# Performance work log

Measured on AMD Instinct MI355X. Metric: run time of the kernel, lower is better.

Reference implementation:

```python
import jax, jax.numpy as jnp
import numpy as np

N_NODES = 10000
N_EDGES = 640000
D_IN = 128
D_MODEL = 128


def _gcn_conv(x, W, b, row, col, norm, n):
    # PyG GCNConv: out = scatter_add(norm * (x W)[row] -> col) + b
    h = x @ W  # [N, d_out]
    msg = h[row] * norm[:, None]  # [E+N, d_out] gather + scale
    out = jax.ops.segment_sum(msg, col, num_segments=n)  # scatter-add
    return out + b


def _norm_with_self_loops(row, col, n):
    # add self loops, compute D^-1/2 (A+I) D^-1/2 edge weights
    loops = jnp.arange(n, dtype=row.dtype)
    row_sl = jnp.concatenate([row, loops])
    col_sl = jnp.concatenate([col, loops])
    deg = jax.ops.segment_sum(jnp.ones_like(col_sl, dtype=jnp.float32), col_sl, num_segments=n)
    dis = jnp.where(deg > 0, jax.lax.rsqrt(jnp.maximum(deg, 1.0)), 0.0)
    norm = dis[row_sl] * dis[col_sl]
    return row_sl, col_sl, norm


def setup_inputs() -> dict:
    key = jax.random.key(0)
    k1, k2, k3, k4 = jax.random.split(key, 4)
    glorot1 = (6.0 / (D_IN + D_MODEL)) ** 0.5
    glorot2 = (6.0 / (D_MODEL + D_MODEL)) ** 0.5
    return {
        "x": jax.random.normal(k1, (N_NODES, D_IN), dtype=jnp.float32),
        "edge_index": jax.random.randint(k2, (2, N_EDGES), 0, N_NODES, dtype=jnp.int32),
        "W1": jax.random.uniform(k3, (D_IN, D_MODEL), jnp.float32, -glorot1, glorot1),
        "b1": jnp.zeros((D_MODEL,), jnp.float32),
        "W2": jax.random.uniform(k4, (D_MODEL, D_MODEL), jnp.float32, -glorot2, glorot2),
        "b2": jnp.zeros((D_MODEL,), jnp.float32),
    }


def reference(x, edge_index, W1, b1, W2, b2):
    n = x.shape[0]
    row, col = edge_index[0], edge_index[1]
    row_sl, col_sl, norm = _norm_with_self_loops(row, col, n)
    x1 = jax.nn.relu(_gcn_conv(x, W1, b1, row_sl, col_sl, norm, n))
    x2 = _gcn_conv(x1, W2, b2, row_sl, col_sl, norm, n)
    return (x2, x1)
```

## Files before the change

### kernel.cpp

```cpp
#include <hip/hip_runtime.h>

#define N_NODES 10000
#define N_EDGES 640000
#define D 128
#define NBUCK 157
#define BSTRIDE 160
#define CAP 4608
#define EPT 20
#define BWG 125

__device__ __forceinline__ float asf(unsigned int u) {
    union { unsigned int i; float f; } v; v.i = u; return v.f;
}
__device__ __forceinline__ unsigned int f2bf(float f) {
    union { float f; unsigned int i; } v; v.f = f;
    return (v.i + 0x7fffu + ((v.i >> 16) & 1u)) >> 16;
}

__global__ __launch_bounds__(256) void k_zero_small(int* __restrict__ slab_cnt,
                                                    int* __restrict__ gcur) {
    int t = threadIdx.x;
    if (t < BSTRIDE) slab_cnt[t] = 0;
    if (t == 0) gcur[0] = 0;
}

__global__ __launch_bounds__(256) void k_bucket(const int* __restrict__ row,
                                                const int* __restrict__ col,
                                                int* __restrict__ slab_cnt,
                                                unsigned int* __restrict__ bucketed) {
    __shared__ int hist[BSTRIDE];
    __shared__ int base_s[BSTRIDE];
    int tid = threadIdx.x;
    if (tid < BSTRIDE) hist[tid] = 0;
    __syncthreads();

    int e0 = blockIdx.x * (256 * EPT) + tid;
    unsigned int word[EPT];
    int rank[EPT];
#pragma unroll
    for (int u = 0; u < EPT; ++u) {
        int e = e0 + u * 256;
        int r = row[e];
        int c = col[e];
        word[u] = (unsigned int)r | ((unsigned int)c << 14);
        rank[u] = atomicAdd(&hist[c >> 6], 1);
    }
    __syncthreads();
    if (tid < NBUCK) base_s[tid] = atomicAdd(&slab_cnt[tid], hist[tid]);
    __syncthreads();
#pragma unroll
    for (int u = 0; u < EPT; ++u) {
        int bkt = (int)(word[u] >> 20);
        int idx = base_s[bkt] + rank[u];
        if (idx < CAP) bucketed[(size_t)bkt * CAP + idx] = word[u];
    }
}

__global__ __launch_bounds__(256) void k_place(const unsigned int* __restrict__ bucketed,
                                               const int* __restrict__ slab_cnt,
                                               int* __restrict__ gcur,
                                               int* __restrict__ sorted_row,
                                               int2* __restrict__ node_be,
                                               float* __restrict__ dis) {
    __shared__ int hist[64];
    __shared__ int start[64];
    __shared__ int cur[64];
    __shared__ int baseS;
    int b = blockIdx.x;
    int tid = threadIdx.x;
    if (tid < 64) hist[tid] = 0;
    __syncthreads();

    int scnt = slab_cnt[b];
    if (scnt > CAP) scnt = CAP;
    const unsigned int* slab = bucketed + (size_t)b * CAP;

    for (int k = tid; k < scnt; k += 256) {
        int cl = (int)(slab[k] >> 14) & 63;
        atomicAdd(&hist[cl], 1);
    }
    __syncthreads();

    if (tid < 64) {
        int v = hist[tid];
        int pre = v;
#pragma unroll
        for (int off = 1; off < 64; off <<= 1) {
            int o = __shfl_up(pre, off);
            if (tid >= off) pre += o;
        }
        start[tid] = pre - v;
        if (tid == 63) baseS = atomicAdd(gcur, pre);
    }
    __syncthreads();
    int base = baseS;
    if (tid < 64) {
        int c = (b << 6) + tid;
        if (c < N_NODES) {
            int beg = base + start[tid];
            node_be[c] = make_int2(beg, beg + hist[tid]);
            dis[c] = rsqrtf((float)(hist[tid] + 1));
        }
        cur[tid] = start[tid];
    }
    __syncthreads();

    for (int k = tid; k < scnt; k += 256) {
        unsigned int w = slab[k];
        int cl = (int)(w >> 14) & 63;
        int r = (int)(w & 0x3FFFu);
        int p = atomicAdd(&cur[cl], 1);
        sorted_row[base + p] = r;
    }
}

#define FMA4(acc, s, w)                    \
    acc.x = fmaf(s, w.x, acc.x);           \
    acc.y = fmaf(s, w.y, acc.y);           \
    acc.z = fmaf(s, w.z, acc.z);           \
    acc.w = fmaf(s, w.w, acc.w);

__global__ __launch_bounds__(256) void k_gemm_scale(const float* __restrict__ in,
                                                    const float* __restrict__ W,
                                                    const float* __restrict__ dis,
                                                    uint2* __restrict__ h2) {
    __shared__ float4 sW[128 * 16];
    const float4* W4 = (const float4*)W;
    int half = blockIdx.x & 1;
    int tile = blockIdx.x >> 1;
    int cx = threadIdx.x;
    int ty = threadIdx.y;
    int tid = ty * 16 + cx;
    for (int i = tid; i < 128 * 16; i += 256) {
        int k = i >> 4, q = i & 15;
        sW[i] = W4[k * 32 + half * 16 + q];
    }
    __syncthreads();

    int r0 = tile * 32 + ty * 2;
    if (r0 >= N_NODES) return;

    const float4* xr = (const float4*)(in + (size_t)r0 * D);
    float4 acc0 = {0, 0, 0, 0}, acc1 = {0, 0, 0, 0};

#pragma unroll 4
    for (int k4 = 0; k4 < 32; ++k4) {
        float4 a0 = xr[k4];
        float4 a1 = xr[32 + k4];
        float4 w;
        w = sW[(k4 * 4 + 0) * 16 + cx];
        FMA4(acc0, a0.x, w) FMA4(acc1, a1.x, w)
        w = sW[(k4 * 4 + 1) * 16 + cx];
        FMA4(acc0, a0.y, w) FMA4(acc1, a1.y, w)
        w = sW[(k4 * 4 + 2) * 16 + cx];
        FMA4(acc0, a0.z, w) FMA4(acc1, a1.z, w)
        w = sW[(k4 * 4 + 3) * 16 + cx];
        FMA4(acc0, a0.w, w) FMA4(acc1, a1.w, w)
    }

#pragma unroll
    for (int j = 0; j < 2; ++j) {
        float ds = dis[r0 + j];
        float4 a = j ? acc1 : acc0;
        uint2 o;
        o.x = f2bf(a.x * ds) | (f2bf(a.y * ds) << 16);
        o.y = f2bf(a.z * ds) | (f2bf(a.w * ds) << 16);
        h2[(size_t)(r0 + j) * 32 + half * 16 + cx] = o;
    }
}

__global__ __launch_bounds__(256) void k_gather(const uint4* __restrict__ h4,
                                                const int2* __restrict__ node_be,
                                                const int* __restrict__ sorted_row,
                                                const float* __restrict__ dis,
                                                const float* __restrict__ b,
                                                float* __restrict__ out, int relu) {
    int wave = threadIdx.x >> 6;
    int lane = threadIdx.x & 63;
    int c = blockIdx.x * 4 + wave;
    int g = lane >> 3;
    int l8 = lane & 7;

    float acc[16];
#pragma unroll
    for (int k = 0; k < 16; ++k) acc[k] = 0.f;

#define LOADROW(r, wa, wb)                                  \
    {                                                       \
        const uint4* p = &h4[(size_t)(r) * 16 + l8 * 2];    \
        wa = p[0]; wb = p[1];                               \
    }
#define ACCUM(wa, wb)                                                    \
    {                                                                    \
        acc[0]  += asf(wa.x << 16); acc[1]  += asf(wa.x & 0xffff0000u);  \
        acc[2]  += asf(wa.y << 16); acc[3]  += asf(wa.y & 0xffff0000u);  \
        acc[4]  += asf(wa.z << 16); acc[5]  += asf(wa.z & 0xffff0000u);  \
        acc[6]  += asf(wa.w << 16); acc[7]  += asf(wa.w & 0xffff0000u);  \
        acc[8]  += asf(wb.x << 16); acc[9]  += asf(wb.x & 0xffff0000u);  \
        acc[10] += asf(wb.y << 16); acc[11] += asf(wb.y & 0xffff0000u);  \
        acc[12] += asf(wb.z << 16); acc[13] += asf(wb.z & 0xffff0000u);  \
        acc[14] += asf(wb.w << 16); acc[15] += asf(wb.w & 0xffff0000u);  \
    }

    if (g == 0) {
        uint4 s0, s1;
        LOADROW(c, s0, s1);
        ACCUM(s0, s1);
    }

    int2 be = node_be[c];
    int end = be.y;
    int j = be.x + g;
    if (j < end) {
        int r_cur = sorted_row[j];
        uint4 c0, c1;
        LOADROW(r_cur, c0, c1);
        int j1 = j + 8;
        int r_nxt = (j1 < end) ? sorted_row[j1] : 0;
        while (j1 < end) {
            int j2 = j1 + 8;
            int r_nn = (j2 < end) ? sorted_row[j2] : 0;
            uint4 n0, n1;
            LOADROW(r_nxt, n0, n1);
            ACCUM(c0, c1);
            c0 = n0; c1 = n1;
            r_nxt = r_nn;
            j1 = j2;
        }
        ACCUM(c0, c1);
    }
#undef LOADROW
#undef ACCUM

#pragma unroll
    for (int k = 0; k < 16; ++k) {
        acc[k] += __shfl_xor(acc[k], 8);
        acc[k] += __shfl_xor(acc[k], 16);
        acc[k] += __shfl_xor(acc[k], 32);
    }

    if (g == 0) {
        float ds = dis[c];
        const float4* b4 = (const float4*)b;
        float4* op = (float4*)(out + (size_t)c * D + l8 * 16);
#pragma unroll
        for (int q = 0; q < 4; ++q) {
            float4 bb = b4[l8 * 4 + q];
            float4 o;
            o.x = fmaf(ds, acc[q * 4 + 0], bb.x);
            o.y = fmaf(ds, acc[q * 4 + 1], bb.y);
            o.z = fmaf(ds, acc[q * 4 + 2], bb.z);
            o.w = fmaf(ds, acc[q * 4 + 3], bb.w);
            if (relu) {
                o.x = fmaxf(o.x, 0.f); o.y = fmaxf(o.y, 0.f);
                o.z = fmaxf(o.z, 0.f); o.w = fmaxf(o.w, 0.f);
            }
            op[q] = o;
        }
    }
}

extern "C" void kernel_launch(void* const* d_in, const int* in_sizes, int n_in,
                              void* d_out, int out_size, void* d_ws, size_t ws_size,
                              hipStream_t stream) {
    const float* x  = (const float*)d_in[0];
    const int*   ei = (const int*)d_in[1];
    const float* W1 = (const float*)d_in[2];
    const float* b1 = (const float*)d_in[3];
    const float* W2 = (const float*)d_in[4];
    const float* b2 = (const float*)d_in[5];

    float* out = (float*)d_out;
    float* x2 = out;
    float* x1 = out + (size_t)N_NODES * D;

    const int* row = ei;
    const int* col = ei + N_EDGES;

    int* slab_cnt       = (int*)d_ws;
    int* gcur           = slab_cnt + BSTRIDE;
    float* dis          = (float*)(gcur + 16);
    int2* node_be       = (int2*)(dis + 10016);
    unsigned int* bucketed = (unsigned int*)(node_be + 10016);
    int* sorted_row     = (int*)(bucketed + (size_t)NBUCK * CAP);
    unsigned int* h     = (unsigned int*)(sorted_row + N_EDGES);

    k_zero_small<<<1, 256, 0, stream>>>(slab_cnt, gcur);
    k_bucket<<<BWG, 256, 0, stream>>>(row, col, slab_cnt, bucketed);
    k_place<<<NBUCK, 256, 0, stream>>>(bucketed, slab_cnt, gcur, sorted_row, node_be, dis);

    k_gemm_scale<<<626, dim3(16, 16), 0, stream>>>(x, W1, dis, (uint2*)h);
    k_gather<<<N_NODES / 4, 256, 0, stream>>>((const uint4*)h, node_be, sorted_row, dis, b1, x1, 1);
    k_gemm_scale<<<626, dim3(16, 16), 0, stream>>>(x1, W2, dis, (uint2*)h);
    k_gather<<<N_NODES / 4, 256, 0, stream>>>((const uint4*)h, node_be, sorted_row, dis, b2, x2, 0);
}
```

Baseline: 152.8 us.

## Fuse CSR build with first GEMM and drop global atomics in bucketing

```diff
diff --git a/kernel.cpp b/kernel.cpp
--- a/kernel.cpp
+++ b/kernel.cpp
@@ -6,8 +6,9 @@
 #define NBUCK 157
 #define BSTRIDE 160
 #define CAP 4608
-#define EPT 20
+#define CAP_BB 80
 #define BWG 125
+#define SLOTS (BWG * CAP_BB)
 
 __device__ __forceinline__ float asf(unsigned int u) {
     union { unsigned int i; float f; } v; v.i = u; return v.f;
@@ -17,100 +18,38 @@
     return (v.i + 0x7fffu + ((v.i >> 16) & 1u)) >> 16;
 }
 
-__global__ __launch_bounds__(256) void k_zero_small(int* __restrict__ slab_cnt,
-                                                    int* __restrict__ gcur) {
-    int t = threadIdx.x;
-    if (t < BSTRIDE) slab_cnt[t] = 0;
-    if (t == 0) gcur[0] = 0;
-}
-
-__global__ __launch_bounds__(256) void k_bucket(const int* __restrict__ row,
-                                                const int* __restrict__ col,
-                                                int* __restrict__ slab_cnt,
+__global__ __launch_bounds__(256) void k_bucket(const int4* __restrict__ row4,
+                                                const int4* __restrict__ col4,
+                                                unsigned short* __restrict__ cnt_bb,
                                                 unsigned int* __restrict__ bucketed) {
     __shared__ int hist[BSTRIDE];
-    __shared__ int base_s[BSTRIDE];
     int tid = threadIdx.x;
     if (tid < BSTRIDE) hist[tid] = 0;
     __syncthreads();
 
-    int e0 = blockIdx.x * (256 * EPT) + tid;
-    unsigned int word[EPT];
-    int rank[EPT];
-#pragma unroll
-    for (int u = 0; u < EPT; ++u) {
-        int e = e0 + u * 256;
-        int r = row[e];
-        int c = col[e];
-        word[u] = (unsigned int)r | ((unsigned int)c << 14);
-        rank[u] = atomicAdd(&hist[c >> 6], 1);
-    }
-    __syncthreads();
-    if (tid < NBUCK) base_s[tid] = atomicAdd(&slab_cnt[tid], hist[tid]);
-    __syncthreads();
-#pragma unroll
-    for (int u = 0; u < EPT; ++u) {
+    int base4 = blockIdx.x * 1280;
+    unsigned int word[20];
+    int rank[20];
+#pragma unroll
+    for (int u = 0; u < 5; ++u) {
+        int4 r = row4[base4 + u * 256 + tid];
+        int4 c = col4[base4 + u * 256 + tid];
+        int e = u * 4;
+        word[e+0] = (unsigned)r.x | ((unsigned)c.x << 14); rank[e+0] = atomicAdd(&hist[c.x >> 6], 1);
+        word[e+1] = (unsigned)r.y | ((unsigned)c.y << 14); rank[e+1] = atomicAdd(&hist[c.y >> 6], 1);
+        word[e+2] = (unsigned)r.z | ((unsigned)c.z << 14); rank[e+2] = atomicAdd(&hist[c.z >> 6], 1);
+        word[e+3] = (unsigned)r.w | ((unsigned)c.w << 14); rank[e+3] = atomicAdd(&hist[c.w >> 6], 1);
+    }
+    __syncthreads();
+    if (tid < NBUCK) {
+        int h = hist[tid];
+        cnt_bb[tid * 128 + blockIdx.x] = (unsigned short)(h < CAP_BB ? h : CAP_BB);
+    }
+#pragma unroll
+    for (int u = 0; u < 20; ++u) {
         int bkt = (int)(word[u] >> 20);
-        int idx = base_s[bkt] + rank[u];
-        if (idx < CAP) bucketed[(size_t)bkt * CAP + idx] = word[u];
-    }
-}
-
-__global__ __launch_bounds__(256) void k_place(const unsigned int* __restrict__ bucketed,
-                                               const int* __restrict__ slab_cnt,
-                                               int* __restrict__ gcur,
-                                               int* __restrict__ sorted_row,
-                                               int2* __restrict__ node_be,
-                                               float* __restrict__ dis) {
-    __shared__ int hist[64];
-    __shared__ int start[64];
-    __shared__ int cur[64];
-    __shared__ int baseS;
-    int b = blockIdx.x;
-    int tid = threadIdx.x;
-    if (tid < 64) hist[tid] = 0;
-    __syncthreads();
-
-    int scnt = slab_cnt[b];
-    if (scnt > CAP) scnt = CAP;
-    const unsigned int* slab = bucketed + (size_t)b * CAP;
-
-    for (int k = tid; k < scnt; k += 256) {
-        int cl = (int)(slab[k] >> 14) & 63;
-        atomicAdd(&hist[cl], 1);
-    }
-    __syncthreads();
-
-    if (tid < 64) {
-        int v = hist[tid];
-        int pre = v;
-#pragma unroll
-        for (int off = 1; off < 64; off <<= 1) {
-            int o = __shfl_up(pre, off);
-            if (tid >= off) pre += o;
-        }
-        start[tid] = pre - v;
-        if (tid == 63) baseS = atomicAdd(gcur, pre);
-    }
-    __syncthreads();
-    int base = baseS;
-    if (tid < 64) {
-        int c = (b << 6) + tid;
-        if (c < N_NODES) {
-            int beg = base + start[tid];
-            node_be[c] = make_int2(beg, beg + hist[tid]);
-            dis[c] = rsqrtf((float)(hist[tid] + 1));
-        }
-        cur[tid] = start[tid];
-    }
-    __syncthreads();
-
-    for (int k = tid; k < scnt; k += 256) {
-        unsigned int w = slab[k];
-        int cl = (int)(w >> 14) & 63;
-        int r = (int)(w & 0x3FFFu);
-        int p = atomicAdd(&cur[cl], 1);
-        sorted_row[base + p] = r;
+        if (rank[u] < CAP_BB)
+            bucketed[(size_t)bkt * SLOTS + blockIdx.x * CAP_BB + rank[u]] = word[u];
     }
 }
 
@@ -120,17 +59,18 @@
     acc.z = fmaf(s, w.z, acc.z);           \
     acc.w = fmaf(s, w.w, acc.w);
 
-__global__ __launch_bounds__(256) void k_gemm_scale(const float* __restrict__ in,
-                                                    const float* __restrict__ W,
-                                                    const float* __restrict__ dis,
-                                                    uint2* __restrict__ h2) {
-    __shared__ float4 sW[128 * 16];
+template <bool SCALE>
+__device__ __forceinline__ void gemm_body(int gb, int tid,
+                                          const float* __restrict__ in,
+                                          const float* __restrict__ W,
+                                          const float* __restrict__ dis,
+                                          uint2* __restrict__ h2,
+                                          float4* sW) {
     const float4* W4 = (const float4*)W;
-    int half = blockIdx.x & 1;
-    int tile = blockIdx.x >> 1;
-    int cx = threadIdx.x;
-    int ty = threadIdx.y;
-    int tid = ty * 16 + cx;
+    int half = gb & 1;
+    int tile = gb >> 1;
+    int cx = tid & 15;
+    int ty = tid >> 4;
     for (int i = tid; i < 128 * 16; i += 256) {
         int k = i >> 4, q = i & 15;
         sW[i] = W4[k * 32 + half * 16 + q];
@@ -142,7 +82,6 @@
 
     const float4* xr = (const float4*)(in + (size_t)r0 * D);
     float4 acc0 = {0, 0, 0, 0}, acc1 = {0, 0, 0, 0};
-
 #pragma unroll 4
     for (int k4 = 0; k4 < 32; ++k4) {
         float4 a0 = xr[k4];
@@ -157,24 +96,95 @@
         w = sW[(k4 * 4 + 3) * 16 + cx];
         FMA4(acc0, a0.w, w) FMA4(acc1, a1.w, w)
     }
-
 #pragma unroll
     for (int j = 0; j < 2; ++j) {
-        float ds = dis[r0 + j];
         float4 a = j ? acc1 : acc0;
         uint2 o;
-        o.x = f2bf(a.x * ds) | (f2bf(a.y * ds) << 16);
-        o.y = f2bf(a.z * ds) | (f2bf(a.w * ds) << 16);
+        if (SCALE) {
+            float ds = dis[r0 + j];
+            o.x = f2bf(a.x * ds) | (f2bf(a.y * ds) << 16);
+            o.y = f2bf(a.z * ds) | (f2bf(a.w * ds) << 16);
+        } else {
+            o.x = f2bf(a.x) | (f2bf(a.y) << 16);
+            o.y = f2bf(a.z) | (f2bf(a.w) << 16);
+        }
         h2[(size_t)(r0 + j) * 32 + half * 16 + cx] = o;
     }
 }
 
+__global__ __launch_bounds__(256) void k_fused1(const unsigned int* __restrict__ bucketed,
+                                                const unsigned short* __restrict__ cnt_bb,
+                                                int* __restrict__ sorted_row,
+                                                int2* __restrict__ node_be,
+                                                float* __restrict__ dis,
+                                                const float* __restrict__ x,
+                                                const float* __restrict__ W1,
+                                                uint2* __restrict__ h2) {
+    __shared__ __align__(16) char smem[32768];
+    int tid = threadIdx.x;
+    if (blockIdx.x >= NBUCK) {
+        gemm_body<false>(blockIdx.x - NBUCK, tid, x, W1, nullptr, h2, (float4*)smem);
+        return;
+    }
+    int* hist = (int*)smem;
+    int* cur  = hist + 64;
+    unsigned short* cnt_l = (unsigned short*)(cur + 64);
+    int b = blockIdx.x;
+    if (tid < 64) hist[tid] = 0;
+    if (tid < BWG) cnt_l[tid] = cnt_bb[b * 128 + tid];
+    __syncthreads();
+
+    const unsigned int* slab = bucketed + (size_t)b * SLOTS;
+    for (int k = tid; k < SLOTS; k += 256) {
+        int blk = k / CAP_BB;
+        int idx = k - blk * CAP_BB;
+        if (idx < (int)cnt_l[blk]) {
+            unsigned int w = slab[k];
+            atomicAdd(&hist[(w >> 14) & 63], 1);
+        }
+    }
+    __syncthreads();
+    if (tid < 64) {
+        int v = hist[tid], pre = v;
+#pragma unroll
+        for (int off = 1; off < 64; off <<= 1) {
+            int o = __shfl_up(pre, off);
+            if (tid >= off) pre += o;
+        }
+        cur[tid] = pre - v;
+        int c = (b << 6) + tid;
+        if (c < N_NODES) {
+            node_be[c] = make_int2(b * CAP + pre - v, b * CAP + pre);
+            dis[c] = rsqrtf((float)(v + 1));
+        }
+    }
+    __syncthreads();
+    for (int k = tid; k < SLOTS; k += 256) {
+        int blk = k / CAP_BB;
+        int idx = k - blk * CAP_BB;
+        if (idx < (int)cnt_l[blk]) {
+            unsigned int w = slab[k];
+            int p = atomicAdd(&cur[(w >> 14) & 63], 1);
+            sorted_row[b * CAP + p] = (int)(w & 0x3FFFu);
+        }
+    }
+}
+
+__global__ __launch_bounds__(256) void k_gemm2(const float* __restrict__ in,
+                                               const float* __restrict__ W,
+                                               const float* __restrict__ dis,
+                                               uint2* __restrict__ h2) {
+    __shared__ __align__(16) float4 sW[128 * 16];
+    gemm_body<true>(blockIdx.x, threadIdx.x, in, W, dis, h2, sW);
+}
+
+template <int MODE>
 __global__ __launch_bounds__(256) void k_gather(const uint4* __restrict__ h4,
                                                 const int2* __restrict__ node_be,
                                                 const int* __restrict__ sorted_row,
                                                 const float* __restrict__ dis,
                                                 const float* __restrict__ b,
-                                                float* __restrict__ out, int relu) {
+                                                float* __restrict__ out) {
     int wave = threadIdx.x >> 6;
     int lane = threadIdx.x & 63;
     int c = blockIdx.x * 4 + wave;
@@ -190,22 +200,31 @@
         const uint4* p = &h4[(size_t)(r) * 16 + l8 * 2];    \
         wa = p[0]; wb = p[1];                               \
     }
-#define ACCUM(wa, wb)                                                    \
-    {                                                                    \
-        acc[0]  += asf(wa.x << 16); acc[1]  += asf(wa.x & 0xffff0000u);  \
-        acc[2]  += asf(wa.y << 16); acc[3]  += asf(wa.y & 0xffff0000u);  \
-        acc[4]  += asf(wa.z << 16); acc[5]  += asf(wa.z & 0xffff0000u);  \
-        acc[6]  += asf(wa.w << 16); acc[7]  += asf(wa.w & 0xffff0000u);  \
-        acc[8]  += asf(wb.x << 16); acc[9]  += asf(wb.x & 0xffff0000u);  \
-        acc[10] += asf(wb.y << 16); acc[11] += asf(wb.y & 0xffff0000u);  \
-        acc[12] += asf(wb.z << 16); acc[13] += asf(wb.z & 0xffff0000u);  \
-        acc[14] += asf(wb.w << 16); acc[15] += asf(wb.w & 0xffff0000u);  \
+#define ACCUMS(wa, wb, s)                                                            \
+    {                                                                                \
+        acc[0]  = fmaf(s, asf(wa.x << 16), acc[0]);                                  \
+        acc[1]  = fmaf(s, asf(wa.x & 0xffff0000u), acc[1]);                          \
+        acc[2]  = fmaf(s, asf(wa.y << 16), acc[2]);                                  \
+        acc[3]  = fmaf(s, asf(wa.y & 0xffff0000u), acc[3]);                          \
+        acc[4]  = fmaf(s, asf(wa.z << 16), acc[4]);                                  \
+        acc[5]  = fmaf(s, asf(wa.z & 0xffff0000u), acc[5]);                          \
+        acc[6]  = fmaf(s, asf(wa.w << 16), acc[6]);                                  \
+        acc[7]  = fmaf(s, asf(wa.w & 0xffff0000u), acc[7]);                          \
+        acc[8]  = fmaf(s, asf(wb.x << 16), acc[8]);                                  \
+        acc[9]  = fmaf(s, asf(wb.x & 0xffff0000u), acc[9]);                          \
+        acc[10] = fmaf(s, asf(wb.y << 16), acc[10]);                                 \
+        acc[11] = fmaf(s, asf(wb.y & 0xffff0000u), acc[11]);                         \
+        acc[12] = fmaf(s, asf(wb.z << 16), acc[12]);                                 \
+        acc[13] = fmaf(s, asf(wb.z & 0xffff0000u), acc[13]);                         \
+        acc[14] = fmaf(s, asf(wb.w << 16), acc[14]);                                 \
+        acc[15] = fmaf(s, asf(wb.w & 0xffff0000u), acc[15]);                         \
     }
 
     if (g == 0) {
         uint4 s0, s1;
         LOADROW(c, s0, s1);
-        ACCUM(s0, s1);
+        float ds = MODE ? dis[c] : 1.0f;
+        ACCUMS(s0, s1, ds);
     }
 
     int2 be = node_be[c];
@@ -215,6 +234,7 @@
         int r_cur = sorted_row[j];
         uint4 c0, c1;
         LOADROW(r_cur, c0, c1);
+        float d_cur = MODE ? dis[r_cur] : 1.0f;
         int j1 = j + 8;
         int r_nxt = (j1 < end) ? sorted_row[j1] : 0;
         while (j1 < end) {
@@ -222,15 +242,16 @@
             int r_nn = (j2 < end) ? sorted_row[j2] : 0;
             uint4 n0, n1;
             LOADROW(r_nxt, n0, n1);
-            ACCUM(c0, c1);
-            c0 = n0; c1 = n1;
+            float d_nxt = MODE ? dis[r_nxt] : 1.0f;
+            ACCUMS(c0, c1, d_cur);
+            c0 = n0; c1 = n1; d_cur = d_nxt;
             r_nxt = r_nn;
             j1 = j2;
         }
-        ACCUM(c0, c1);
+        ACCUMS(c0, c1, d_cur);
     }
 #undef LOADROW
-#undef ACCUM
+#undef ACCUMS
 
 #pragma unroll
     for (int k = 0; k < 16; ++k) {
@@ -251,7 +272,7 @@
             o.y = fmaf(ds, acc[q * 4 + 1], bb.y);
             o.z = fmaf(ds, acc[q * 4 + 2], bb.z);
             o.w = fmaf(ds, acc[q * 4 + 3], bb.w);
-            if (relu) {
+            if (MODE) {
                 o.x = fmaxf(o.x, 0.f); o.y = fmaxf(o.y, 0.f);
                 o.z = fmaxf(o.z, 0.f); o.w = fmaxf(o.w, 0.f);
             }
@@ -274,23 +295,21 @@
     float* x2 = out;
     float* x1 = out + (size_t)N_NODES * D;
 
-    const int* row = ei;
-    const int* col = ei + N_EDGES;
-
-    int* slab_cnt       = (int*)d_ws;
-    int* gcur           = slab_cnt + BSTRIDE;
-    float* dis          = (float*)(gcur + 16);
-    int2* node_be       = (int2*)(dis + 10016);
-    unsigned int* bucketed = (unsigned int*)(node_be + 10016);
-    int* sorted_row     = (int*)(bucketed + (size_t)NBUCK * CAP);
-    unsigned int* h     = (unsigned int*)(sorted_row + N_EDGES);
-
-    k_zero_small<<<1, 256, 0, stream>>>(slab_cnt, gcur);
-    k_bucket<<<BWG, 256, 0, stream>>>(row, col, slab_cnt, bucketed);
-    k_place<<<NBUCK, 256, 0, stream>>>(bucketed, slab_cnt, gcur, sorted_row, node_be, dis);
-
-    k_gemm_scale<<<626, dim3(16, 16), 0, stream>>>(x, W1, dis, (uint2*)h);
-    k_gather<<<N_NODES / 4, 256, 0, stream>>>((const uint4*)h, node_be, sorted_row, dis, b1, x1, 1);
-    k_gemm_scale<<<626, dim3(16, 16), 0, stream>>>(x1, W2, dis, (uint2*)h);
-    k_gather<<<N_NODES / 4, 256, 0, stream>>>((const uint4*)h, node_be, sorted_row, dis, b2, x2, 0);
-}
+    const int4* row4 = (const int4*)ei;
+    const int4* col4 = (const int4*)(ei + N_EDGES);
+
+    char* w = (char*)d_ws;
+    unsigned short* cnt_bb = (unsigned short*)w;            w += 157 * 128 * 2;
+    float* dis             = (float*)w;                     w += 10016 * 4;
+    int2* node_be          = (int2*)w;                      w += 10016 * 8;
+    unsigned int* bucketed = (unsigned int*)w;              w += (size_t)NBUCK * SLOTS * 4;
+    int* sorted_row        = (int*)w;                       w += (size_t)NBUCK * CAP * 4;
+    unsigned int* h        = (unsigned int*)w;
+
+    k_bucket<<<BWG, 256, 0, stream>>>(row4, col4, cnt_bb, bucketed);
+    k_fused1<<<NBUCK + 626, 256, 0, stream>>>(bucketed, cnt_bb, sorted_row, node_be, dis,
+                                              x, W1, (uint2*)h);
+    k_gather<1><<<N_NODES / 4, 256, 0, stream>>>((const uint4*)h, node_be, sorted_row, dis, b1, x1);
+    k_gemm2<<<626, 256, 0, stream>>>(x1, W2, dis, (uint2*)h);
+    k_gather<0><<<N_NODES / 4, 256, 0, stream>>>((const uint4*)h, node_be, sorted_row, dis, b2, x2);
+}
```

Result: faster. 148.1 us (-3.1%).
